# Optimization experiments

Hardware: AMD Instinct MI355X
Metric: run time of the kernel (lower is better)

Reference implementation:

```python
import jax, jax.numpy as jnp
import numpy as np

N_NODES = 50000
N_EDGES = 800000
N_IN = 96
N_HID = 96
N_CLS = 16
P_DROP = 0.5


def setup_inputs() -> dict:
    key = jax.random.key(0)
    ks = jax.random.split(key, 10)
    return {
        "features": jax.random.normal(ks[0], (N_NODES, N_IN), dtype=jnp.float32),
        "edge_weight": jax.random.uniform(ks[1], (N_EDGES,), dtype=jnp.float32),
        "src": jax.random.randint(ks[2], (N_EDGES,), 0, N_NODES),
        "dst": jax.random.randint(ks[3], (N_EDGES,), 0, N_NODES),
        "W0": jax.random.normal(ks[4], (N_IN, N_HID), dtype=jnp.float32) / np.sqrt(N_IN).astype(np.float32),
        "b0": jnp.zeros((N_HID,), dtype=jnp.float32),
        "W1": jax.random.normal(ks[5], (N_HID, N_HID), dtype=jnp.float32) / np.sqrt(N_HID).astype(np.float32),
        "b1": jnp.zeros((N_HID,), dtype=jnp.float32),
        "W2": jax.random.normal(ks[6], (N_HID, N_CLS), dtype=jnp.float32) / np.sqrt(N_HID).astype(np.float32),
        "b2": jnp.zeros((N_CLS,), dtype=jnp.float32),
    }


def reference(features, edge_weight, src, dst, W0, b0, W1, b1, W2, b2):
    N = features.shape[0]
    # Unweighted node degrees (DGL GraphConv norm='both'), clamped to >= 1.
    ones_e = jnp.ones_like(edge_weight)
    out_deg = jnp.clip(jax.ops.segment_sum(ones_e, src, num_segments=N), 1.0)
    in_deg = jnp.clip(jax.ops.segment_sum(ones_e, dst, num_segments=N), 1.0)
    inv_sqrt_out = out_deg ** -0.5  # [N]
    inv_sqrt_in = in_deg ** -0.5    # [N]

    def graph_conv(h, W, b, act):
        h = h * inv_sqrt_out[:, None]
        m = h[src] * edge_weight[:, None]                   # [E, d] gather + edge scale
        agg = jax.ops.segment_sum(m, dst, num_segments=N)   # [N, d] scatter-add
        out = (agg * inv_sqrt_in[:, None]) @ W + b          # D_in^-1/2, then linear + bias
        return act(out) if act is not None else out

    layers = [(W0, b0, jax.nn.relu), (W1, b1, jax.nn.relu), (W2, b2, None)]
    dkey = jax.random.key(42)
    h = features
    for i, (W, b, act) in enumerate(layers):
        keep = jax.random.bernoulli(jax.random.fold_in(dkey, i), 1.0 - P_DROP, h.shape)
        h = jnp.where(keep, h / (1.0 - P_DROP), 0.0)        # dropout p=0.5
        h = graph_conv(h, W, b, act)
    return jax.nn.log_softmax(h, axis=1)
```

## Files before the change

kernel.cpp:

```cpp
#include <hip/hip_runtime.h>
#include <hip/hip_fp16.h>
#include <stdint.h>

#define NNODES 50000
#define NEDGES 800000
#define NHID 96
#define NCLS 16

#define NC 100
#define NR 4
#define EPB (NEDGES / NC)
#define RNODES (NNODES / NR)
#define RWORDS8 (RNODES / 4)
#define NWORDS8 (NNODES / 4)
#define SCANB ((NWORDS8 + 255) / 256)
#define HISTBLKS (NC * NR)
#define FEPT 4
#define FILLB2 ((NEDGES / FEPT + 255) / 256)
#define NDROP4 ((NNODES * NHID / 4 + 255) / 256)

__host__ __device__ inline void tf2x32(uint32_t k0, uint32_t k1, uint32_t x0, uint32_t x1,
                                       uint32_t& o0, uint32_t& o1) {
  uint32_t k2 = k0 ^ k1 ^ 0x1BD11BDAu;
#define TFROT(v, r) (((v) << (r)) | ((v) >> (32 - (r))))
#define TFR(r) { x0 += x1; x1 = TFROT(x1, r); x1 ^= x0; }
  x0 += k0; x1 += k1;
  TFR(13) TFR(15) TFR(26) TFR(6)
  x0 += k1; x1 += k2 + 1u;
  TFR(17) TFR(29) TFR(16) TFR(24)
  x0 += k2; x1 += k0 + 2u;
  TFR(13) TFR(15) TFR(26) TFR(6)
  x0 += k0; x1 += k1 + 3u;
  TFR(17) TFR(29) TFR(16) TFR(24)
  x0 += k1; x1 += k2 + 4u;
  TFR(13) TFR(15) TFR(26) TFR(6)
  x0 += k2; x1 += k0 + 5u;
  o0 = x0; o1 = x1;
#undef TFR
#undef TFROT
}

__device__ inline bool keep_bit(uint32_t k0, uint32_t k1, uint32_t j) {
  uint32_t o0, o1;
  tf2x32(k0, k1, 0u, j, o0, o1);
  return (((o0 ^ o1) >> 31) == 0u);
}

__global__ __launch_bounds__(256) void hist_kernel(
    const int* __restrict__ src, const int* __restrict__ dst,
    uint32_t* __restrict__ slabD, uint32_t* __restrict__ slabS,
    uint8_t* __restrict__ rank8, uint32_t* __restrict__ flags) {
  __shared__ uint32_t HD[RWORDS8];
  __shared__ uint32_t HS[RWORDS8];
  const int tid = threadIdx.x, b = blockIdx.x;
  if (b == 0 && tid < SCANB) flags[tid] = 0;
  const int c = b / NR, r = b - c * NR;
  const int e0 = c * EPB, e1 = e0 + EPB;
  const int nbase = r * RNODES;
  for (int w = tid; w < RWORDS8; w += 256) { HD[w] = 0; HS[w] = 0; }
  __syncthreads();
  int e = e0 + tid;
  for (; e + 768 < e1; e += 1024) {
    int d0 = dst[e] - nbase,       d1 = dst[e + 256] - nbase;
    int d2 = dst[e + 512] - nbase, d3 = dst[e + 768] - nbase;
    int s0 = src[e] - nbase,       s1 = src[e + 256] - nbase;
    int s2 = src[e + 512] - nbase, s3 = src[e + 768] - nbase;
    if ((unsigned)d0 < (unsigned)RNODES) {
      int sh = (d0 & 3) * 8;
      uint32_t old = atomicAdd(&HD[d0 >> 2], 1u << sh);
      rank8[e] = (uint8_t)((old >> sh) & 0xFFu);
    }
    if ((unsigned)d1 < (unsigned)RNODES) {
      int sh = (d1 & 3) * 8;
      uint32_t old = atomicAdd(&HD[d1 >> 2], 1u << sh);
      rank8[e + 256] = (uint8_t)((old >> sh) & 0xFFu);
    }
    if ((unsigned)d2 < (unsigned)RNODES) {
      int sh = (d2 & 3) * 8;
      uint32_t old = atomicAdd(&HD[d2 >> 2], 1u << sh);
      rank8[e + 512] = (uint8_t)((old >> sh) & 0xFFu);
    }
    if ((unsigned)d3 < (unsigned)RNODES) {
      int sh = (d3 & 3) * 8;
      uint32_t old = atomicAdd(&HD[d3 >> 2], 1u << sh);
      rank8[e + 768] = (uint8_t)((old >> sh) & 0xFFu);
    }
    if ((unsigned)s0 < (unsigned)RNODES) atomicAdd(&HS[s0 >> 2], 1u << ((s0 & 3) * 8));
    if ((unsigned)s1 < (unsigned)RNODES) atomicAdd(&HS[s1 >> 2], 1u << ((s1 & 3) * 8));
    if ((unsigned)s2 < (unsigned)RNODES) atomicAdd(&HS[s2 >> 2], 1u << ((s2 & 3) * 8));
    if ((unsigned)s3 < (unsigned)RNODES) atomicAdd(&HS[s3 >> 2], 1u << ((s3 & 3) * 8));
  }
  for (; e < e1; e += 256) {
    int d = dst[e] - nbase;
    if ((unsigned)d < (unsigned)RNODES) {
      int sh = (d & 3) * 8;
      uint32_t old = atomicAdd(&HD[d >> 2], 1u << sh);
      rank8[e] = (uint8_t)((old >> sh) & 0xFFu);
    }
    int s = src[e] - nbase;
    if ((unsigned)s < (unsigned)RNODES) atomicAdd(&HS[s >> 2], 1u << ((s & 3) * 8));
  }
  __syncthreads();
  uint32_t* dpD = slabD + (size_t)b * RWORDS8;
  uint32_t* dpS = slabS + (size_t)b * RWORDS8;
  for (int w = tid; w < RWORDS8; w += 256) { dpD[w] = HD[w]; dpS[w] = HS[w]; }
}

__global__ __launch_bounds__(256) void reduce_scan_kernel(
    const uint32_t* __restrict__ slabD, const uint32_t* __restrict__ slabS,
    float* __restrict__ inv_o, float* __restrict__ inv_i,
    uint32_t* __restrict__ rel8, int* __restrict__ row_ptr,
    uint32_t* __restrict__ flags) {
  __shared__ int lds[256];
  __shared__ int base_s;
  const int tid = threadIdx.x, b = blockIdx.x;
  const int gw = b * 256 + tid;
  uint32_t runD = 0, runS = 0;
  int n0 = 0;
  if (gw < NWORDS8) {
    int r = gw / RWORDS8, lw = gw - r * RWORDS8;
    n0 = r * RNODES + 4 * lw;
#pragma unroll 4
    for (int c = 0; c < NC; ++c) {
      rel8[(size_t)c * NWORDS8 + gw] = runD;
      runD += slabD[(size_t)(c * NR + r) * RWORDS8 + lw];
      runS += slabS[(size_t)(c * NR + r) * RWORDS8 + lw];
    }
  }
  const int d0 = runD & 0xFF, d1 = (runD >> 8) & 0xFF,
            d2 = (runD >> 16) & 0xFF, d3 = runD >> 24;
  const int tsum = d0 + d1 + d2 + d3;
  lds[tid] = tsum;
  __syncthreads();
  for (int off = 1; off < 256; off <<= 1) {
    int t = (tid >= off) ? lds[tid - off] : 0;
    __syncthreads();
    lds[tid] += t;
    __syncthreads();
  }
  const int incl = lds[tid];
  if (tid == 255) atomicExch(&flags[b], 0x80000000u | (uint32_t)lds[255]);
  if (tid < 64) {
    uint32_t part = 0;
    if (tid < b) {
      uint32_t v;
      do { v = atomicAdd(&flags[tid], 0u); } while (!(v & 0x80000000u));
      part = v & 0x7FFFFFFFu;
    }
#pragma unroll
    for (int off = 32; off > 0; off >>= 1)
      part += __shfl_down((unsigned)part, off, 64);
    if (tid == 0) base_s = (int)part;
  }
  __syncthreads();
  const int base = base_s;
  if (gw < NWORDS8) {
    int excl = base + incl - tsum;
    *(int4*)(row_ptr + n0) = make_int4(excl, excl + d0, excl + d0 + d1, excl + d0 + d1 + d2);
    *(float4*)(inv_i + n0) = make_float4(
        rsqrtf(fmaxf((float)d0, 1.0f)), rsqrtf(fmaxf((float)d1, 1.0f)),
        rsqrtf(fmaxf((float)d2, 1.0f)), rsqrtf(fmaxf((float)d3, 1.0f)));
    int o0 = runS & 0xFF, o1 = (runS >> 8) & 0xFF, o2 = (runS >> 16) & 0xFF, o3 = runS >> 24;
    *(float4*)(inv_o + n0) = make_float4(
        rsqrtf(fmaxf((float)o0, 1.0f)), rsqrtf(fmaxf((float)o1, 1.0f)),
        rsqrtf(fmaxf((float)o2, 1.0f)), rsqrtf(fmaxf((float)o3, 1.0f)));
    if (gw == NWORDS8 - 1) row_ptr[NNODES] = NEDGES;
  }
}

__global__ __launch_bounds__(256) void fill_drop_kernel(
    const int* __restrict__ src, const int* __restrict__ dst, const float* __restrict__ ew,
    const uint8_t* __restrict__ rank8, const uint32_t* __restrict__ rel8,
    const int* __restrict__ row_ptr, uint32_t* __restrict__ csr,
    const float* __restrict__ h, const float* __restrict__ inv_o,
    float* __restrict__ X, uint32_t k0, uint32_t k1) {
  const int bi = blockIdx.x;
  if (bi < FILLB2) {
    int t = bi * 256 + threadIdx.x;
    int e = t * 4;
    if (e >= NEDGES) return;
    int4 d4 = *(const int4*)(dst + e);
    int4 s4 = *(const int4*)(src + e);
    float4 w4 = *(const float4*)(ew + e);
    uint32_t r4 = *(const uint32_t*)(rank8 + e);
    const uint32_t* rel = rel8 + (size_t)(e / EPB) * NWORDS8;
#pragma unroll
    for (int k = 0; k < 4; ++k) {
      int d = (&d4.x)[k];
      int s = (&s4.x)[k];
      float w = (&w4.x)[k];
      int rk = (int)((r4 >> (k * 8)) & 0xFFu);
      int sh = (d & 3) * 8;
      int rel_v = (int)((rel[d >> 2] >> sh) & 0xFFu);
      int pos = row_ptr[d] + rel_v + rk;
      uint32_t v = ((uint32_t)s << 16) | (uint32_t)__half_as_ushort(__float2half_rn(w));
      if ((unsigned)pos < (unsigned)NEDGES) csr[pos] = v;
    }
    return;
  }
  int j = ((bi - FILLB2) * 256 + threadIdx.x) * 4;
  if (j < NNODES * NHID) {
    int n = j / NHID;
    float4 hv = *(const float4*)(h + j);
    float sc = 2.0f * inv_o[n];
    float4 o;
    o.x = keep_bit(k0, k1, (uint32_t)(j + 0)) ? hv.x * sc : 0.0f;
    o.y = keep_bit(k0, k1, (uint32_t)(j + 1)) ? hv.y * sc : 0.0f;
    o.z = keep_bit(k0, k1, (uint32_t)(j + 2)) ? hv.z * sc : 0.0f;
    o.w = keep_bit(k0, k1, (uint32_t)(j + 3)) ? hv.w * sc : 0.0f;
    *(float4*)(X + j) = o;
  }
}

__global__ __launch_bounds__(256) void gemm96_kernel(
    const float* __restrict__ X, const float* __restrict__ W, __half* __restrict__ Yh) {
  __shared__ float Wl[96 * 96];
  const int tid = threadIdx.x;
  {
    const float4* Wg = (const float4*)W;
    float4* Ws = (float4*)Wl;
#pragma unroll
    for (int i = 0; i < 9; ++i)
      Ws[tid + i * 256] = Wg[tid + i * 256];
  }
  __syncthreads();

  const int cg = tid & 7;
  const int rq = tid >> 3;
  const int row0 = blockIdx.x * 128 + rq * 4;
  const int c0 = cg * 12;

  float acc[4][12];
#pragma unroll
  for (int r = 0; r < 4; ++r)
#pragma unroll
    for (int c = 0; c < 12; ++c) acc[r][c] = 0.f;

  const float* xr[4];
#pragma unroll
  for (int r = 0; r < 4; ++r) {
    int rr = row0 + r; if (rr > NNODES - 1) rr = NNODES - 1;
    xr[r] = X + (size_t)rr * 96;
  }

  for (int k = 0; k < 96; k += 4) {
    float4 x4[4];
#pragma unroll
    for (int r = 0; r < 4; ++r) x4[r] = *(const float4*)(xr[r] + k);
#pragma unroll
    for (int kk = 0; kk < 4; ++kk) {
      const float4* wp = (const float4*)(Wl + (k + kk) * 96 + c0);
      float4 w0 = wp[0], w1 = wp[1], w2 = wp[2];
      float xv[4] = { (&x4[0].x)[kk], (&x4[1].x)[kk], (&x4[2].x)[kk], (&x4[3].x)[kk] };
#pragma unroll
      for (int r = 0; r < 4; ++r) {
        acc[r][0]  += xv[r] * w0.x; acc[r][1]  += xv[r] * w0.y;
        acc[r][2]  += xv[r] * w0.z; acc[r][3]  += xv[r] * w0.w;
        acc[r][4]  += xv[r] * w1.x; acc[r][5]  += xv[r] * w1.y;
        acc[r][6]  += xv[r] * w1.z; acc[r][7]  += xv[r] * w1.w;
        acc[r][8]  += xv[r] * w2.x; acc[r][9]  += xv[r] * w2.y;
        acc[r][10] += xv[r] * w2.z; acc[r][11] += xv[r] * w2.w;
      }
    }
  }

#pragma unroll
  for (int r = 0; r < 4; ++r) {
    int rr = row0 + r;
    if (rr < NNODES) {
      __half2* hp = (__half2*)(Yh + (size_t)rr * 96 + c0);
#pragma unroll
      for (int c = 0; c < 6; ++c)
        hp[c] = __floats2half2_rn(acc[r][2 * c], acc[r][2 * c + 1]);
    }
  }
}

__global__ __launch_bounds__(256) void gemm16_kernel(
    const float* __restrict__ X, const float* __restrict__ W, __half* __restrict__ Y2h) {
  __shared__ float Wl[96 * 16];
  const int tid = threadIdx.x;
  {
    const float4* Wg = (const float4*)W;
    float4* Ws = (float4*)Wl;
    for (int i = tid; i < 384; i += 256) Ws[i] = Wg[i];
  }
  __syncthreads();

  const int row0 = blockIdx.x * 512 + tid * 2;
  const float* xr[2];
#pragma unroll
  for (int r = 0; r < 2; ++r) {
    int rr = row0 + r; if (rr > NNODES - 1) rr = NNODES - 1;
    xr[r] = X + (size_t)rr * 96;
  }

  float acc[2][16];
#pragma unroll
  for (int r = 0; r < 2; ++r)
#pragma unroll
    for (int c = 0; c < 16; ++c) acc[r][c] = 0.f;

  for (int k = 0; k < 96; k += 4) {
    float4 x4[2];
#pragma unroll
    for (int r = 0; r < 2; ++r) x4[r] = *(const float4*)(xr[r] + k);
#pragma unroll
    for (int kk = 0; kk < 4; ++kk) {
      const float4* wp = (const float4*)(Wl + (k + kk) * 16);
      float4 w0 = wp[0], w1 = wp[1], w2 = wp[2], w3 = wp[3];
#pragma unroll
      for (int r = 0; r < 2; ++r) {
        float xv = (&x4[r].x)[kk];
        acc[r][0]  += xv * w0.x; acc[r][1]  += xv * w0.y;
        acc[r][2]  += xv * w0.z; acc[r][3]  += xv * w0.w;
        acc[r][4]  += xv * w1.x; acc[r][5]  += xv * w1.y;
        acc[r][6]  += xv * w1.z; acc[r][7]  += xv * w1.w;
        acc[r][8]  += xv * w2.x; acc[r][9]  += xv * w2.y;
        acc[r][10] += xv * w2.z; acc[r][11] += xv * w2.w;
        acc[r][12] += xv * w3.x; acc[r][13] += xv * w3.y;
        acc[r][14] += xv * w3.z; acc[r][15] += xv * w3.w;
      }
    }
  }

#pragma unroll
  for (int r = 0; r < 2; ++r) {
    int rr = row0 + r;
    if (rr < NNODES) {
      __half2* hp = (__half2*)(Y2h + (size_t)rr * 16);
#pragma unroll
      for (int c = 0; c < 8; ++c)
        hp[c] = __floats2half2_rn(acc[r][2 * c], acc[r][2 * c + 1]);
    }
  }
}

#define ACC8(u0, wt) { \
  float2 g0 = __half22float2(*(__half2*)&u0.x); \
  float2 g1 = __half22float2(*(__half2*)&u0.y); \
  float2 g2 = __half22float2(*(__half2*)&u0.z); \
  float2 g3 = __half22float2(*(__half2*)&u0.w); \
  acc[0] += g0.x * wt; acc[1] += g0.y * wt; \
  acc[2] += g1.x * wt; acc[3] += g1.y * wt; \
  acc[4] += g2.x * wt; acc[5] += g2.y * wt; \
  acc[6] += g3.x * wt; acc[7] += g3.y * wt; }

__global__ __launch_bounds__(256) void gather96_drop_kernel(
    const __half* __restrict__ Yh, const uint32_t* __restrict__ csr,
    const int* __restrict__ row_ptr, const float* __restrict__ inv_in,
    const float* __restrict__ inv_o, const float* __restrict__ bias,
    float* __restrict__ Xn, uint32_t k0, uint32_t k1) {
  int tid = blockIdx.x * 256 + threadIdx.x;
  int n = tid / 12;
  int q = tid - n * 12;
  if (n >= NNODES) return;
  int beg = row_ptr[n], end = row_ptr[n + 1];
  float acc[8];
#pragma unroll
  for (int i = 0; i < 8; ++i) acc[i] = 0.f;

  int p = beg;
  for (; p + 8 <= end; p += 8) {
    uint32_t pw[8];
#pragma unroll
    for (int i = 0; i < 8; ++i) pw[i] = csr[p + i];
    float wv[8];
    uint4 u[8];
#pragma unroll
    for (int i = 0; i < 8; ++i) {
      int s = (int)(pw[i] >> 16); if (s >= NNODES) s = 0;
      wv[i] = __half2float(__ushort_as_half((unsigned short)(pw[i] & 0xFFFFu)));
      u[i] = *(const uint4*)(Yh + (size_t)s * 96 + q * 8);
    }
#pragma unroll
    for (int i = 0; i < 8; ++i) { ACC8(u[i], wv[i]) }
  }
  for (; p + 2 <= end; p += 2) {
    uint32_t pa = csr[p], pb = csr[p + 1];
    int s0 = pa >> 16, s1 = pb >> 16;
    if (s0 >= NNODES) s0 = 0;
    if (s1 >= NNODES) s1 = 0;
    float w0 = __half2float(__ushort_as_half((unsigned short)(pa & 0xFFFFu)));
    float w1 = __half2float(__ushort_as_half((unsigned short)(pb & 0xFFFFu)));
    uint4 a0 = *(const uint4*)(Yh + (size_t)s0 * 96 + q * 8);
    uint4 b0 = *(const uint4*)(Yh + (size_t)s1 * 96 + q * 8);
    ACC8(a0, w0)
    ACC8(b0, w1)
  }
  if (p < end) {
    uint32_t pa = csr[p];
    int s0 = pa >> 16;
    if (s0 >= NNODES) s0 = 0;
    float w0 = __half2float(__ushort_as_half((unsigned short)(pa & 0xFFFFu)));
    uint4 a0 = *(const uint4*)(Yh + (size_t)s0 * 96 + q * 8);
    ACC8(a0, w0)
  }

  float iv = inv_in[n];
  float sc = 2.0f * inv_o[n];
  const float* bp = bias + q * 8;
  float o[8];
#pragma unroll
  for (int i = 0; i < 8; ++i)
    o[i] = fmaxf(acc[i] * iv + bp[i], 0.f) * sc;
  uint32_t jb = (uint32_t)(n * 96 + q * 8);
#pragma unroll
  for (int i = 0; i < 8; ++i)
    o[i] = keep_bit(k0, k1, jb + i) ? o[i] : 0.f;
  float* xp = Xn + (size_t)n * 96 + q * 8;
  *(float4*)(xp + 0) = make_float4(o[0], o[1], o[2], o[3]);
  *(float4*)(xp + 4) = make_float4(o[4], o[5], o[6], o[7]);
}

__global__ __launch_bounds__(256) void gather16_lsm_kernel(
    const __half* __restrict__ Y2h, const uint32_t* __restrict__ csr,
    const int* __restrict__ row_ptr, const float* __restrict__ inv_in,
    const float* __restrict__ b2, float* __restrict__ out) {
  int t = blockIdx.x * 256 + threadIdx.x;
  int n = t >> 1;
  int q = t & 1;
  if (n >= NNODES) return;
  int beg = row_ptr[n], end = row_ptr[n + 1];
  float acc[8];
#pragma unroll
  for (int i = 0; i < 8; ++i) acc[i] = 0.f;

  int p = beg;
  for (; p + 4 <= end; p += 4) {
    uint32_t pa = csr[p], pb = csr[p + 1], pc = csr[p + 2], pd = csr[p + 3];
    int sa = pa >> 16, sb = pb >> 16, sc_ = pc >> 16, sd = pd >> 16;
    if (sa >= NNODES) sa = 0;
    if (sb >= NNODES) sb = 0;
    if (sc_ >= NNODES) sc_ = 0;
    if (sd >= NNODES) sd = 0;
    float wa = __half2float(__ushort_as_half((unsigned short)(pa & 0xFFFFu)));
    float wb = __half2float(__ushort_as_half((unsigned short)(pb & 0xFFFFu)));
    float wc = __half2float(__ushort_as_half((unsigned short)(pc & 0xFFFFu)));
    float wd = __half2float(__ushort_as_half((unsigned short)(pd & 0xFFFFu)));
    uint4 a0 = *(const uint4*)(Y2h + (size_t)sa * 16 + q * 8);
    uint4 b0 = *(const uint4*)(Y2h + (size_t)sb * 16 + q * 8);
    uint4 c0 = *(const uint4*)(Y2h + (size_t)sc_ * 16 + q * 8);
    uint4 d0 = *(const uint4*)(Y2h + (size_t)sd * 16 + q * 8);
    ACC8(a0, wa) ACC8(b0, wb) ACC8(c0, wc) ACC8(d0, wd)
  }
  for (; p + 2 <= end; p += 2) {
    uint32_t pa = csr[p], pb = csr[p + 1];
    int sa = pa >> 16, sb = pb >> 16;
    if (sa >= NNODES) sa = 0;
    if (sb >= NNODES) sb = 0;
    float wa = __half2float(__ushort_as_half((unsigned short)(pa & 0xFFFFu)));
    float wb = __half2float(__ushort_as_half((unsigned short)(pb & 0xFFFFu)));
    uint4 a0 = *(const uint4*)(Y2h + (size_t)sa * 16 + q * 8);
    uint4 b0 = *(const uint4*)(Y2h + (size_t)sb * 16 + q * 8);
    ACC8(a0, wa) ACC8(b0, wb)
  }
  if (p < end) {
    uint32_t pa = csr[p];
    int sa = pa >> 16;
    if (sa >= NNODES) sa = 0;
    float wa = __half2float(__ushort_as_half((unsigned short)(pa & 0xFFFFu)));
    uint4 a0 = *(const uint4*)(Y2h + (size_t)sa * 16 + q * 8);
    ACC8(a0, wa)
  }

  float iv = inv_in[n];
  float v[8];
#pragma unroll
  for (int i = 0; i < 8; ++i) v[i] = acc[i] * iv + b2[q * 8 + i];
  float m = v[0];
#pragma unroll
  for (int i = 1; i < 8; i++) m = fmaxf(m, v[i]);
  m = fmaxf(m, __shfl_xor(m, 1));
  float s = 0.f;
#pragma unroll
  for (int i = 0; i < 8; i++) s += expf(v[i] - m);
  s += __shfl_xor(s, 1);
  float ls = logf(s);
  float* orow = out + (size_t)n * 16 + q * 8;
  *(float4*)(orow + 0) = make_float4(v[0] - m - ls, v[1] - m - ls, v[2] - m - ls, v[3] - m - ls);
  *(float4*)(orow + 4) = make_float4(v[4] - m - ls, v[5] - m - ls, v[6] - m - ls, v[7] - m - ls);
}

extern "C" void kernel_launch(void* const* d_in, const int* in_sizes, int n_in,
                              void* d_out, int out_size, void* d_ws, size_t ws_size,
                              hipStream_t stream) {
  const float* feat = (const float*)d_in[0];
  const float* ew   = (const float*)d_in[1];
  const int*   src  = (const int*)d_in[2];
  const int*   dst  = (const int*)d_in[3];
  const float* W0   = (const float*)d_in[4];
  const float* b0   = (const float*)d_in[5];
  const float* W1   = (const float*)d_in[6];
  const float* b1   = (const float*)d_in[7];
  const float* W2   = (const float*)d_in[8];
  const float* b2   = (const float*)d_in[9];
  float* out = (float*)d_out;

  char* base = (char*)d_ws;
  size_t off = 0;
  auto take = [&](size_t nbytes) {
    void* q = base + off;
    off += (nbytes + 255) & ~(size_t)255;
    return q;
  };
  uint32_t* flags   = (uint32_t*)take((size_t)SCANB * 4);
  int*      row_ptr = (int*)take((size_t)(NNODES + 1) * 4);
  float*    inv_o   = (float*)take((size_t)NNODES * 4);
  float*    inv_i   = (float*)take((size_t)NNODES * 4);
  uint32_t* slabD   = (uint32_t*)take((size_t)NC * NR * RWORDS8 * 4);
  uint32_t* slabS   = (uint32_t*)take((size_t)NC * NR * RWORDS8 * 4);
  uint32_t* rel8    = (uint32_t*)take((size_t)NC * NWORDS8 * 4);
  uint8_t*  rank8   = (uint8_t*)take((size_t)NEDGES);
  uint32_t* csr     = (uint32_t*)take((size_t)NEDGES * 4);
  float*    X       = (float*)take((size_t)NNODES * NHID * 4);
  __half*   Yh      = (__half*)take((size_t)NNODES * NHID * 2);
  __half*   Y2h     = (__half*)take((size_t)NNODES * NCLS * 2);
  (void)ws_size; (void)in_sizes; (void)n_in; (void)out_size;

  uint32_t k[3][2];
  for (uint32_t i = 0; i < 3; i++) tf2x32(0u, 42u, 0u, i, k[i][0], k[i][1]);

  hist_kernel<<<HISTBLKS, 256, 0, stream>>>(src, dst, slabD, slabS, rank8, flags);
  reduce_scan_kernel<<<SCANB, 256, 0, stream>>>(slabD, slabS, inv_o, inv_i, rel8, row_ptr, flags);
  fill_drop_kernel<<<FILLB2 + NDROP4, 256, 0, stream>>>(
      src, dst, ew, rank8, rel8, row_ptr, csr, feat, inv_o, X, k[0][0], k[0][1]);

  const int G96  = (NNODES + 127) / 128;
  const int G16  = (NNODES + 511) / 512;
  const int GGD  = (NNODES * 12 + 255) / 256;
  const int GLSM = (NNODES * 2 + 255) / 256;

  gemm96_kernel<<<G96, 256, 0, stream>>>(X, W0, Yh);
  gather96_drop_kernel<<<GGD, 256, 0, stream>>>(Yh, csr, row_ptr, inv_i, inv_o, b0, X, k[1][0], k[1][1]);
  gemm96_kernel<<<G96, 256, 0, stream>>>(X, W1, Yh);
  gather96_drop_kernel<<<GGD, 256, 0, stream>>>(Yh, csr, row_ptr, inv_i, inv_o, b1, X, k[2][0], k[2][1]);
  gemm16_kernel<<<G16, 256, 0, stream>>>(X, W2, Y2h);
  gather16_lsm_kernel<<<GLSM, 256, 0, stream>>>(Y2h, csr, row_ptr, inv_i, b2, out);
}
```

Measured before the change: 263.9 us.

## Fold out-degree normalization into CSR edge weights; move layer-0 dropout into hist kernel

The D_out^-1/2 source scaling now goes into each CSR edge weight (ew * inv_o[src]) when the CSR is filled, not into the node features. Because the dropout of layer 0 no longer needs inv_o, it can run inside the histogram kernel as extra blocks, overlapping with degree counting. That lightens the fill kernel and drops one load per node from the gather epilogues. The risk is precision: the fp16 edge weight now carries the product, and fill_kernel does an extra random gather of inv_o[s].

```diff
diff --git a/kernel.cpp b/kernel.cpp
--- a/kernel.cpp
+++ b/kernel.cpp
@@ -46,13 +46,28 @@
   return (((o0 ^ o1) >> 31) == 0u);
 }
 
-__global__ __launch_bounds__(256) void hist_kernel(
+__global__ __launch_bounds__(256) void hist_drop_kernel(
     const int* __restrict__ src, const int* __restrict__ dst,
     uint32_t* __restrict__ slabD, uint32_t* __restrict__ slabS,
-    uint8_t* __restrict__ rank8, uint32_t* __restrict__ flags) {
+    uint8_t* __restrict__ rank8, uint32_t* __restrict__ flags,
+    const float* __restrict__ h, float* __restrict__ X,
+    uint32_t k0, uint32_t k1) {
   __shared__ uint32_t HD[RWORDS8];
   __shared__ uint32_t HS[RWORDS8];
   const int tid = threadIdx.x, b = blockIdx.x;
+  if (b >= HISTBLKS) {
+    int j = ((b - HISTBLKS) * 256 + tid) * 4;
+    if (j < NNODES * NHID) {
+      float4 hv = *(const float4*)(h + j);
+      float4 o;
+      o.x = keep_bit(k0, k1, (uint32_t)(j + 0)) ? hv.x * 2.0f : 0.0f;
+      o.y = keep_bit(k0, k1, (uint32_t)(j + 1)) ? hv.y * 2.0f : 0.0f;
+      o.z = keep_bit(k0, k1, (uint32_t)(j + 2)) ? hv.z * 2.0f : 0.0f;
+      o.w = keep_bit(k0, k1, (uint32_t)(j + 3)) ? hv.w * 2.0f : 0.0f;
+      *(float4*)(X + j) = o;
+    }
+    return;
+  }
   if (b == 0 && tid < SCANB) flags[tid] = 0;
   const int c = b / NR, r = b - c * NR;
   const int e0 = c * EPB, e1 = e0 + EPB;
@@ -168,47 +183,30 @@
   }
 }
 
-__global__ __launch_bounds__(256) void fill_drop_kernel(
+__global__ __launch_bounds__(256) void fill_kernel(
     const int* __restrict__ src, const int* __restrict__ dst, const float* __restrict__ ew,
     const uint8_t* __restrict__ rank8, const uint32_t* __restrict__ rel8,
-    const int* __restrict__ row_ptr, uint32_t* __restrict__ csr,
-    const float* __restrict__ h, const float* __restrict__ inv_o,
-    float* __restrict__ X, uint32_t k0, uint32_t k1) {
-  const int bi = blockIdx.x;
-  if (bi < FILLB2) {
-    int t = bi * 256 + threadIdx.x;
-    int e = t * 4;
-    if (e >= NEDGES) return;
-    int4 d4 = *(const int4*)(dst + e);
-    int4 s4 = *(const int4*)(src + e);
-    float4 w4 = *(const float4*)(ew + e);
-    uint32_t r4 = *(const uint32_t*)(rank8 + e);
-    const uint32_t* rel = rel8 + (size_t)(e / EPB) * NWORDS8;
-#pragma unroll
-    for (int k = 0; k < 4; ++k) {
-      int d = (&d4.x)[k];
-      int s = (&s4.x)[k];
-      float w = (&w4.x)[k];
-      int rk = (int)((r4 >> (k * 8)) & 0xFFu);
-      int sh = (d & 3) * 8;
-      int rel_v = (int)((rel[d >> 2] >> sh) & 0xFFu);
-      int pos = row_ptr[d] + rel_v + rk;
-      uint32_t v = ((uint32_t)s << 16) | (uint32_t)__half_as_ushort(__float2half_rn(w));
-      if ((unsigned)pos < (unsigned)NEDGES) csr[pos] = v;
-    }
-    return;
-  }
-  int j = ((bi - FILLB2) * 256 + threadIdx.x) * 4;
-  if (j < NNODES * NHID) {
-    int n = j / NHID;
-    float4 hv = *(const float4*)(h + j);
-    float sc = 2.0f * inv_o[n];
-    float4 o;
-    o.x = keep_bit(k0, k1, (uint32_t)(j + 0)) ? hv.x * sc : 0.0f;
-    o.y = keep_bit(k0, k1, (uint32_t)(j + 1)) ? hv.y * sc : 0.0f;
-    o.z = keep_bit(k0, k1, (uint32_t)(j + 2)) ? hv.z * sc : 0.0f;
-    o.w = keep_bit(k0, k1, (uint32_t)(j + 3)) ? hv.w * sc : 0.0f;
-    *(float4*)(X + j) = o;
+    const int* __restrict__ row_ptr, const float* __restrict__ inv_o,
+    uint32_t* __restrict__ csr) {
+  int t = blockIdx.x * 256 + threadIdx.x;
+  int e = t * 4;
+  if (e >= NEDGES) return;
+  int4 d4 = *(const int4*)(dst + e);
+  int4 s4 = *(const int4*)(src + e);
+  float4 w4 = *(const float4*)(ew + e);
+  uint32_t r4 = *(const uint32_t*)(rank8 + e);
+  const uint32_t* rel = rel8 + (size_t)(e / EPB) * NWORDS8;
+#pragma unroll
+  for (int k = 0; k < 4; ++k) {
+    int d = (&d4.x)[k];
+    int s = (&s4.x)[k];
+    float w = (&w4.x)[k] * inv_o[s];
+    int rk = (int)((r4 >> (k * 8)) & 0xFFu);
+    int sh = (d & 3) * 8;
+    int rel_v = (int)((rel[d >> 2] >> sh) & 0xFFu);
+    int pos = row_ptr[d] + rel_v + rk;
+    uint32_t v = ((uint32_t)s << 16) | (uint32_t)__half_as_ushort(__float2half_rn(w));
+    if ((unsigned)pos < (unsigned)NEDGES) csr[pos] = v;
   }
 }
 
@@ -349,7 +347,7 @@
 __global__ __launch_bounds__(256) void gather96_drop_kernel(
     const __half* __restrict__ Yh, const uint32_t* __restrict__ csr,
     const int* __restrict__ row_ptr, const float* __restrict__ inv_in,
-    const float* __restrict__ inv_o, const float* __restrict__ bias,
+    const float* __restrict__ bias,
     float* __restrict__ Xn, uint32_t k0, uint32_t k1) {
   int tid = blockIdx.x * 256 + threadIdx.x;
   int n = tid / 12;
@@ -398,12 +396,11 @@
   }
 
   float iv = inv_in[n];
-  float sc = 2.0f * inv_o[n];
   const float* bp = bias + q * 8;
   float o[8];
 #pragma unroll
   for (int i = 0; i < 8; ++i)
-    o[i] = fmaxf(acc[i] * iv + bp[i], 0.f) * sc;
+    o[i] = fmaxf(acc[i] * iv + bp[i], 0.f) * 2.0f;
   uint32_t jb = (uint32_t)(n * 96 + q * 8);
 #pragma unroll
   for (int i = 0; i < 8; ++i)
@@ -521,10 +518,10 @@
   uint32_t k[3][2];
   for (uint32_t i = 0; i < 3; i++) tf2x32(0u, 42u, 0u, i, k[i][0], k[i][1]);
 
-  hist_kernel<<<HISTBLKS, 256, 0, stream>>>(src, dst, slabD, slabS, rank8, flags);
+  hist_drop_kernel<<<HISTBLKS + NDROP4, 256, 0, stream>>>(
+      src, dst, slabD, slabS, rank8, flags, feat, X, k[0][0], k[0][1]);
   reduce_scan_kernel<<<SCANB, 256, 0, stream>>>(slabD, slabS, inv_o, inv_i, rel8, row_ptr, flags);
-  fill_drop_kernel<<<FILLB2 + NDROP4, 256, 0, stream>>>(
-      src, dst, ew, rank8, rel8, row_ptr, csr, feat, inv_o, X, k[0][0], k[0][1]);
+  fill_kernel<<<FILLB2, 256, 0, stream>>>(src, dst, ew, rank8, rel8, row_ptr, inv_o, csr);
 
   const int G96  = (NNODES + 127) / 128;
   const int G16  = (NNODES + 511) / 512;
@@ -532,9 +529,9 @@
   const int GLSM = (NNODES * 2 + 255) / 256;
 
   gemm96_kernel<<<G96, 256, 0, stream>>>(X, W0, Yh);
-  gather96_drop_kernel<<<GGD, 256, 0, stream>>>(Yh, csr, row_ptr, inv_i, inv_o, b0, X, k[1][0], k[1][1]);
+  gather96_drop_kernel<<<GGD, 256, 0, stream>>>(Yh, csr, row_ptr, inv_i, b0, X, k[1][0], k[1][1]);
   gemm96_kernel<<<G96, 256, 0, stream>>>(X, W1, Yh);
-  gather96_drop_kernel<<<GGD, 256, 0, stream>>>(Yh, csr, row_ptr, inv_i, inv_o, b1, X, k[2][0], k[2][1]);
+  gather96_drop_kernel<<<GGD, 256, 0, stream>>>(Yh, csr, row_ptr, inv_i, b1, X, k[2][0], k[2][1]);
   gemm16_kernel<<<G16, 256, 0, stream>>>(X, W2, Y2h);
   gather16_lsm_kernel<<<GLSM, 256, 0, stream>>>(Y2h, csr, row_ptr, inv_i, b2, out);
 }
```

Measured after the change: 265.5 us. Within noise of the previous version (+0.6%).
